# Optimization experiments

Measured on AMD Instinct MI355X. Metric: run time of the kernel, lower is better.

The kernel has to match this reference:

```python
import jax, jax.numpy as jnp
import numpy as np

N_NODES = 32768
N_EDGES = 524288
NODE_DIM = 128
HIDDEN = 256
EDGE_DIM = 32


def setup_inputs() -> dict:
    key = jax.random.key(0)
    ks = jax.random.split(key, 12)
    s = 0.05
    return {
        "h": jax.random.normal(ks[0], (N_NODES, NODE_DIM), jnp.float32),
        "x": jax.random.normal(ks[1], (N_NODES, 3), jnp.float32) * 10.0,
        "edge_index": jax.random.randint(ks[2], (2, N_EDGES), 0, N_NODES, dtype=jnp.int32).astype(jnp.int64),
        "edge_dist": jax.random.uniform(ks[3], (N_EDGES,), jnp.float32) * 15.0,
        # edge_mlp: Linear(1, edge_dim) -> SiLU -> Linear(edge_dim, edge_dim)
        "We1": jax.random.normal(ks[4], (1, EDGE_DIM), jnp.float32) * s,
        "be1": jnp.zeros((EDGE_DIM,), jnp.float32),
        "We2": jax.random.normal(ks[5], (EDGE_DIM, EDGE_DIM), jnp.float32) * s,
        "be2": jnp.zeros((EDGE_DIM,), jnp.float32),
        # node_mlp: Linear(2*node+edge, hidden) -> SiLU -> Linear(hidden, node)
        "Wn1": jax.random.normal(ks[6], (2 * NODE_DIM + EDGE_DIM, HIDDEN), jnp.float32) * s,
        "bn1": jnp.zeros((HIDDEN,), jnp.float32),
        "Wn2": jax.random.normal(ks[7], (HIDDEN, NODE_DIM), jnp.float32) * s,
        "bn2": jnp.zeros((NODE_DIM,), jnp.float32),
        # coord_mlp: Linear(2*node+edge, hidden) -> SiLU -> Linear(hidden, 1, bias=False)
        "Wc1": jax.random.normal(ks[8], (2 * NODE_DIM + EDGE_DIM, HIDDEN), jnp.float32) * s,
        "bc1": jnp.zeros((HIDDEN,), jnp.float32),
        "Wc2": jax.random.normal(ks[9], (HIDDEN, 1), jnp.float32) * s,
    }


def reference(h, x, edge_index, edge_dist,
              We1, be1, We2, be2,
              Wn1, bn1, Wn2, bn2,
              Wc1, bc1, Wc2):
    src, dst = edge_index[0], edge_index[1]
    n_nodes = h.shape[0]

    # edge_mlp on scalar distances -> [E, edge_dim]
    edge_attr = jax.nn.silu(edge_dist[:, None] @ We1 + be1) @ We2 + be2

    # per-edge message input: [E, 2*node_dim + edge_dim]
    m_input = jnp.concatenate([h[src], h[dst], edge_attr], axis=-1)

    # node messages and scatter-add onto destination nodes
    m = jax.nn.silu(m_input @ Wn1 + bn1) @ Wn2 + bn2          # [E, node_dim]
    h_agg = jax.ops.segment_sum(m, dst, num_segments=n_nodes)  # [N, node_dim]

    # equivariant coordinate update along normalized edge direction
    coord_weight = jax.nn.silu(m_input @ Wc1 + bc1) @ Wc2      # [E, 1]
    dir_vec = x[src] - x[dst]                                  # [E, 3]
    dir_len = jnp.maximum(jnp.linalg.norm(dir_vec, axis=-1, keepdims=True), 1e-8)
    coord_update = coord_weight * (dir_vec / dir_len)          # [E, 3]
    x_agg = jax.ops.segment_sum(coord_update, dst, num_segments=n_nodes)

    return h + h_agg, x + x_agg
```

## Files before the change

### kernel.cpp

```cpp
#include <hip/hip_runtime.h>
#include <math.h>

#define N_NODES 32768
#define N_EDGES 524288
#define NODE_DIM 128
#define HIDDEN 256
#define EDGE_DIM 32
#define TE 32
#define NBLK (N_EDGES / TE)
#define ASTR 296
#define HSTR 264
#define MSTR 132

typedef __attribute__((ext_vector_type(8))) short bf16x8;
typedef __attribute__((ext_vector_type(16))) float f32x16;

__device__ __forceinline__ float silu_f(float v) {
    float e = __expf(-v);
    return v * __builtin_amdgcn_rcpf(1.0f + e);
}

__device__ __forceinline__ unsigned short f2bf_rne(float f) {
    union { float f; unsigned int u; } v; v.f = f;
    return (unsigned short)((v.u + 0x7fffu + ((v.u >> 16) & 1u)) >> 16);
}
__device__ __forceinline__ unsigned int pk_rne(float a, float b) {
    return (unsigned int)f2bf_rne(a) | ((unsigned int)f2bf_rne(b) << 16);
}
__device__ __forceinline__ unsigned int pkbf(float a, float b) {
    union { float f; unsigned int u; } ua, ub; ua.f = a; ub.f = b;
    return __builtin_amdgcn_perm(ub.u + 0x8000u, ua.u + 0x8000u, 0x07060302u);
}
__device__ __forceinline__ unsigned short f2bf_hu(float f) {
    union { float f; unsigned int u; } v; v.f = f;
    return (unsigned short)((v.u + 0x8000u) >> 16);
}

__device__ __forceinline__ int detect_is64(const void* ei, int t) {
    const unsigned int* ew = (const unsigned int*)ei;
    unsigned int hiw = ew[2 * (t & 63) + 1];
    return (__ballot(hiw != 0u) == 0ULL) ? 1 : 0;
}

#define WS_BIAS_OFF 1024
#define WS_W1S_OFF  69632
#define WS_W2S_OFF  364544
#define WS_CNT_OFF  430080
#define WS_CUR_OFF  561152
#define WS_PERM_OFF 692224
#define WS_PART_OFF 2789376
#define WS_HBF_OFF  2790400
#define WS_HBF_END  (WS_HBF_OFF + N_NODES * NODE_DIM * 2)

#define SEG_CNT  32768
#define SEG_W1S  147456
#define SEG_W2S  32768
#define SEG_BIAS 512
#define SEG_OUT  1073152
#define SEG_HBF  524288
#define PREP_TOT (SEG_CNT + SEG_W1S + SEG_W2S + SEG_BIAS + SEG_OUT + SEG_HBF)

__global__ void prep_all_kernel(const float* __restrict__ h, const float* __restrict__ x,
                                const float* __restrict__ We2, const float* __restrict__ be2,
                                const float* __restrict__ Wn1, const float* __restrict__ bn1,
                                const float* __restrict__ Wn2,
                                const float* __restrict__ Wc1, const float* __restrict__ bc1,
                                float* __restrict__ out, float* __restrict__ biasC,
                                unsigned short* __restrict__ W1s, unsigned short* __restrict__ W2s,
                                int* __restrict__ counts, unsigned short* __restrict__ hbf) {
    int i = blockIdx.x * 256 + threadIdx.x;
    if (i < SEG_CNT) { counts[i] = 0; return; }
    i -= SEG_CNT;
    if (i < SEG_W1S) {
        int jj = i & 7, ln = (i >> 3) & 63, rest = i >> 9;
        int step = rest % 18, tile = rest / 18;
        int n = tile * 32 + (ln & 31);
        int k = step * 16 + ((ln >> 5) * 8) + jj;
        float v;
        if (k < 256) {
            v = (n < 256) ? Wn1[k * 256 + n] : Wc1[k * 256 + (n - 256)];
        } else {
            int j = k - 256;
            float s = 0.0f;
            #pragma unroll 8
            for (int q = 0; q < 32; ++q)
                s += We2[j * 32 + q] * ((n < 256) ? Wn1[(256 + q) * 256 + n]
                                                  : Wc1[(256 + q) * 256 + (n - 256)]);
            v = s;
        }
        W1s[i] = f2bf_rne(v);
        return;
    }
    i -= SEG_W1S;
    if (i < SEG_W2S) {
        int jj = i & 7, ln = (i >> 3) & 63, rest = i >> 9;
        int step = rest & 15, tile = rest >> 4;
        int d = tile * 32 + (ln & 31);
        int k = step * 16 + ((ln >> 5) * 8) + jj;
        W2s[i] = f2bf_rne(Wn2[k * 128 + d]);
        return;
    }
    i -= SEG_W2S;
    if (i < SEG_BIAS) {
        int n = i;
        float s = (n < 256) ? bn1[n] : bc1[n - 256];
        #pragma unroll 8
        for (int q = 0; q < 32; ++q)
            s += be2[q] * ((n < 256) ? Wn1[(256 + q) * 256 + n]
                                     : Wc1[(256 + q) * 256 + (n - 256)]);
        biasC[n] = s;
        return;
    }
    i -= SEG_BIAS;
    if (i < SEG_OUT) {
        const int NH4 = N_NODES * NODE_DIM / 4;
        const float4* h4 = (const float4*)h;
        const float4* x4 = (const float4*)x;
        ((float4*)out)[i] = (i < NH4) ? h4[i] : x4[i - NH4];
        return;
    }
    i -= SEG_OUT;
    if (hbf != nullptr && i < SEG_HBF) {
        const float4* p = (const float4*)&h[i * 8];
        float4 v0 = p[0], v1 = p[1];
        uint4 o = make_uint4(pk_rne(v0.x, v0.y), pk_rne(v0.z, v0.w),
                             pk_rne(v1.x, v1.y), pk_rne(v1.z, v1.w));
        *(uint4*)&hbf[i * 8] = o;
    }
}

__global__ void hist_kernel(const void* __restrict__ ei, int* __restrict__ counts) {
    int is64 = detect_is64(ei, threadIdx.x);
    int e = blockIdx.x * 256 + threadIdx.x;
    int dst = is64 ? (int)((const long long*)ei)[N_EDGES + e]
                   : ((const int*)ei)[N_EDGES + e];
    atomicAdd(&counts[dst], 1);
}

__global__ __launch_bounds__(256)
void scanA_kernel(const int* __restrict__ counts, int* __restrict__ partials) {
    __shared__ int red[256];
    const int t = threadIdx.x;
    const int b = blockIdx.x;
    red[t] = counts[b * 256 + t];
    __syncthreads();
    #pragma unroll
    for (int s = 128; s > 0; s >>= 1) {
        if (t < s) red[t] += red[t + s];
        __syncthreads();
    }
    if (t == 0) partials[b] = red[0];
}

__global__ __launch_bounds__(256)
void scanC_kernel(const int* __restrict__ counts, const int* __restrict__ partials,
                  int* __restrict__ cursor) {
    __shared__ int pb[128];
    __shared__ int loc[256];
    const int t = threadIdx.x;
    const int b = blockIdx.x;
    if (t < 128) pb[t] = partials[t];
    int c = counts[b * 256 + t];
    loc[t] = c;
    __syncthreads();
    if (t == 0) {
        int s = 0;
        for (int j = 0; j < 128; ++j) { int v = pb[j]; pb[j] = s; s += v; }
    }
    #pragma unroll
    for (int d = 1; d < 256; d <<= 1) {
        int v = (t >= d) ? loc[t - d] : 0;
        __syncthreads();
        loc[t] += v;
        __syncthreads();
    }
    cursor[b * 256 + t] = pb[b] + loc[t] - c;
}

__global__ void place_kernel(const void* __restrict__ ei,
                             int* __restrict__ cursor, int* __restrict__ perm) {
    int is64 = detect_is64(ei, threadIdx.x);
    int e = blockIdx.x * 256 + threadIdx.x;
    int dst = is64 ? (int)((const long long*)ei)[N_EDGES + e]
                   : ((const int*)ei)[N_EDGES + e];
    int pos = atomicAdd(&cursor[dst], 1);
    perm[pos] = e;
}

__global__ __launch_bounds__(256, 5)
void egnn_mfma_kernel(const float* __restrict__ h, const float* __restrict__ x,
                      const void* __restrict__ ei, const float* __restrict__ dist,
                      const float* __restrict__ We1, const float* __restrict__ be1,
                      const float* __restrict__ bn2, const float* __restrict__ Wc2,
                      const float* __restrict__ biasC,
                      const unsigned short* __restrict__ W1s,
                      const unsigned short* __restrict__ W2s,
                      const int* __restrict__ perm,
                      const unsigned short* __restrict__ hbf,
                      float* __restrict__ out)
{
    __shared__ unsigned short smA[TE * ASTR];
    __shared__ int sidx[TE], didx[TE], eidx[TE];
    __shared__ float cw_s[TE];
    __shared__ float cxyz[3 * TE];

    unsigned short* smH = smA;
    float* smM = (float*)smA;

    const int t = threadIdx.x;
    const int lane = t & 63;
    const int wv = t >> 6;
    const int lo = lane & 31;
    const int hi = lane >> 5;
    const int swz = ((blockIdx.x & 7) * (NBLK / 8)) + (blockIdx.x >> 3);
    const int ebase = swz * TE;
    const int is64 = detect_is64(ei, t);

    if (t < 2 * TE) {
        int e = t & (TE - 1);
        int eid = perm[ebase + e];
        int which = t >> 5;
        long long pos = (long long)which * N_EDGES + eid;
        int idx = is64 ? (int)((const long long*)ei)[pos] : ((const int*)ei)[pos];
        if (which == 0) { sidx[e] = idx; eidx[e] = eid; }
        else didx[e] = idx;
        if (t < TE) cw_s[t] = 0.0f;
    }
    __syncthreads();

    if (hbf != nullptr) {
        #pragma unroll
        for (int it = 0; it < 4; ++it) {
            int id = it * 256 + t;
            int g = id & 15;
            int half = (id >> 4) & 1;
            int e = id >> 5;
            int node = half ? didx[e] : sidx[e];
            uint4 v = *(const uint4*)&hbf[node * NODE_DIM + 8 * g];
            *(uint4*)&smA[e * ASTR + half * NODE_DIM + 8 * g] = v;
        }
    } else {
        #pragma unroll
        for (int it = 0; it < 4; ++it) {
            int id = it * 256 + t;
            int g8 = id & 15;
            int half = (id >> 4) & 1;
            int e = id >> 5;
            int node = half ? didx[e] : sidx[e];
            const float4* p = (const float4*)&h[node * NODE_DIM + 8 * g8];
            float4 v0 = p[0], v1 = p[1];
            unsigned int a0 = pkbf(v0.x, v0.y), a1 = pkbf(v0.z, v0.w);
            unsigned int a2 = pkbf(v1.x, v1.y), a3 = pkbf(v1.z, v1.w);
            *(uint4*)&smA[e * ASTR + half * NODE_DIM + 8 * g8] = make_uint4(a0, a1, a2, a3);
        }
    }
    {
        int e = t >> 3;
        int j4 = (t & 7) * 4;
        float d = dist[eidx[e]];
        float s0 = silu_f(d * We1[j4 + 0] + be1[j4 + 0]);
        float s1 = silu_f(d * We1[j4 + 1] + be1[j4 + 1]);
        float s2 = silu_f(d * We1[j4 + 2] + be1[j4 + 2]);
        float s3 = silu_f(d * We1[j4 + 3] + be1[j4 + 3]);
        *(uint2*)&smA[e * ASTR + 2 * NODE_DIM + j4] = make_uint2(pkbf(s0, s1), pkbf(s2, s3));
    }
    if (t < TE) {
        int s = sidx[t], dn = didx[t];
        float dx = x[s * 3 + 0] - x[dn * 3 + 0];
        float dy = x[s * 3 + 1] - x[dn * 3 + 1];
        float dz = x[s * 3 + 2] - x[dn * 3 + 2];
        float len = fmaxf(sqrtf(dx * dx + dy * dy + dz * dz), 1e-8f);
        float inv = 1.0f / len;
        cxyz[t] = dx * inv; cxyz[TE + t] = dy * inv; cxyz[2 * TE + t] = dz * inv;
    }
    __syncthreads();

    const int rowbase = 4 * hi;

    {
        f32x16 c0, c1;
        {
            float b0 = biasC[256 + wv * 32 + lo];
            float b1 = biasC[256 + (wv + 4) * 32 + lo];
            #pragma unroll
            for (int r = 0; r < 16; ++r) { c0[r] = b0; c1[r] = b1; }
        }
        {
            const int ao = lo * ASTR + hi * 8;
            const int TS = 18 * 64 * 8;
            const int q0 = (8 + wv) * TS + lane * 8;
            const int q1 = (12 + wv) * TS + lane * 8;
            bf16x8 p0[2], p1[2];
            p0[0] = *(const bf16x8*)&W1s[q0];
            p1[0] = *(const bf16x8*)&W1s[q1];
            #pragma unroll
            for (int step = 0; step < 18; ++step) {
                const int cur = step & 1, nxt = cur ^ 1;
                if (step + 1 < 18) {
                    p0[nxt] = *(const bf16x8*)&W1s[q0 + (step + 1) * 512];
                    p1[nxt] = *(const bf16x8*)&W1s[q1 + (step + 1) * 512];
                }
                bf16x8 f = *(const bf16x8*)&smA[ao + step * 16];
                c0 = __builtin_amdgcn_mfma_f32_32x32x16_bf16(f, p0[cur], c0, 0, 0, 0);
                c1 = __builtin_amdgcn_mfma_f32_32x32x16_bf16(f, p1[cur], c1, 0, 0, 0);
            }
        }
        float w0 = Wc2[wv * 32 + lo];
        float w1 = Wc2[(wv + 4) * 32 + lo];
        float p[16];
        #pragma unroll
        for (int r = 0; r < 16; ++r)
            p[r] = silu_f(c0[r]) * w0 + silu_f(c1[r]) * w1;
        #pragma unroll
        for (int off = 1; off < 32; off <<= 1) {
            #pragma unroll
            for (int r = 0; r < 16; ++r) p[r] += __shfl_xor(p[r], off);
        }
        if (lo == 0) {
            #pragma unroll
            for (int r = 0; r < 16; ++r)
                atomicAdd(&cw_s[(r & 3) + 8 * (r >> 2) + rowbase], p[r]);
        }
    }

    f32x16 a0, a1;
    {
        float b0 = biasC[wv * 32 + lo];
        float b1 = biasC[(wv + 4) * 32 + lo];
        #pragma unroll
        for (int r = 0; r < 16; ++r) { a0[r] = b0; a1[r] = b1; }
        const int ao = lo * ASTR + hi * 8;
        const int TS = 18 * 64 * 8;
        const int q0 = (wv) * TS + lane * 8;
        const int q1 = (wv + 4) * TS + lane * 8;
        bf16x8 p0[2], p1[2];
        p0[0] = *(const bf16x8*)&W1s[q0];
        p1[0] = *(const bf16x8*)&W1s[q1];
        #pragma unroll
        for (int step = 0; step < 18; ++step) {
            const int cur = step & 1, nxt = cur ^ 1;
            if (step + 1 < 18) {
                p0[nxt] = *(const bf16x8*)&W1s[q0 + (step + 1) * 512];
                p1[nxt] = *(const bf16x8*)&W1s[q1 + (step + 1) * 512];
            }
            bf16x8 f = *(const bf16x8*)&smA[ao + step * 16];
            a0 = __builtin_amdgcn_mfma_f32_32x32x16_bf16(f, p0[cur], a0, 0, 0, 0);
            a1 = __builtin_amdgcn_mfma_f32_32x32x16_bf16(f, p1[cur], a1, 0, 0, 0);
        }
    }
    __syncthreads();

    {
        const int jb0 = (wv    ) * 32 + lo;
        const int jb1 = (wv + 4) * 32 + lo;
        #pragma unroll
        for (int r = 0; r < 16; ++r) {
            int er = (r & 3) + 8 * (r >> 2) + rowbase;
            smH[er * HSTR + jb0] = f2bf_hu(silu_f(a0[r]));
            smH[er * HSTR + jb1] = f2bf_hu(silu_f(a1[r]));
        }
    }
    if (t < TE) {
        float w = cw_s[t];
        cxyz[t] *= w; cxyz[TE + t] *= w; cxyz[2 * TE + t] *= w;
    }
    __syncthreads();

    {
        const int d = wv * 32 + lo;
        f32x16 acc;
        float bb = bn2[d];
        #pragma unroll
        for (int r = 0; r < 16; ++r) acc[r] = bb;
        const int hoff = lo * HSTR + hi * 8;
        const int wb = wv * (16 * 64 * 8) + lane * 8;
        bf16x8 bs[2];
        bs[0] = *(const bf16x8*)&W2s[wb];
        #pragma unroll
        for (int step = 0; step < 16; ++step) {
            const int cur = step & 1, nxt = cur ^ 1;
            if (step + 1 < 16)
                bs[nxt] = *(const bf16x8*)&W2s[wb + (step + 1) * 512];
            bf16x8 af = *(const bf16x8*)&smH[hoff + step * 16];
            acc = __builtin_amdgcn_mfma_f32_32x32x16_bf16(af, bs[cur], acc, 0, 0, 0);
        }
        __syncthreads();
        #pragma unroll
        for (int r = 0; r < 16; ++r) {
            int er = (r & 3) + 8 * (r >> 2) + rowbase;
            smM[er * MSTR + d] = acc[r];
        }
    }
    __syncthreads();

    {
        const int g = t >> 5;
        const int d4 = (t & 31) * 4;
        for (int e0 = g; e0 < TE; e0 += 8) {
            if (e0 > 0 && didx[e0] == didx[e0 - 1]) continue;
            float4 s = *(const float4*)&smM[e0 * MSTR + d4];
            int er = e0 + 1;
            while (er < TE && didx[er] == didx[e0]) {
                float4 v = *(const float4*)&smM[er * MSTR + d4];
                s.x += v.x; s.y += v.y; s.z += v.z; s.w += v.w;
                ++er;
            }
            float* dp = &out[didx[e0] * NODE_DIM + d4];
            if (e0 > 0 && er < TE) {
                float4 cur = *(const float4*)dp;
                cur.x += s.x; cur.y += s.y; cur.z += s.z; cur.w += s.w;
                *(float4*)dp = cur;
            } else {
                atomicAdd(dp + 0, s.x); atomicAdd(dp + 1, s.y);
                atomicAdd(dp + 2, s.z); atomicAdd(dp + 3, s.w);
            }
        }
    }
    if (t < TE) {
        int e0 = t;
        if (e0 == 0 || didx[e0] != didx[e0 - 1]) {
            float sx = cxyz[e0], sy = cxyz[TE + e0], sz = cxyz[2 * TE + e0];
            int er = e0 + 1;
            while (er < TE && didx[er] == didx[e0]) {
                sx += cxyz[er]; sy += cxyz[TE + er]; sz += cxyz[2 * TE + er];
                ++er;
            }
            float* xo = out + N_NODES * NODE_DIM + didx[e0] * 3;
            if (e0 > 0 && er < TE) {
                xo[0] += sx; xo[1] += sy; xo[2] += sz;
            } else {
                atomicAdd(xo + 0, sx); atomicAdd(xo + 1, sy); atomicAdd(xo + 2, sz);
            }
        }
    }
}

extern "C" void kernel_launch(void* const* d_in, const int* in_sizes, int n_in,
                              void* d_out, int out_size, void* d_ws, size_t ws_size,
                              hipStream_t stream) {
    const float* h    = (const float*)d_in[0];
    const float* x    = (const float*)d_in[1];
    const void*  ei   = d_in[2];
    const float* dist = (const float*)d_in[3];
    const float* We1  = (const float*)d_in[4];
    const float* be1  = (const float*)d_in[5];
    const float* We2  = (const float*)d_in[6];
    const float* be2  = (const float*)d_in[7];
    const float* Wn1  = (const float*)d_in[8];
    const float* bn1  = (const float*)d_in[9];
    const float* Wn2  = (const float*)d_in[10];
    const float* bn2  = (const float*)d_in[11];
    const float* Wc1  = (const float*)d_in[12];
    const float* bc1  = (const float*)d_in[13];
    const float* Wc2  = (const float*)d_in[14];
    float* out = (float*)d_out;

    float* biasC = (float*)((char*)d_ws + WS_BIAS_OFF);
    unsigned short* W1s = (unsigned short*)((char*)d_ws + WS_W1S_OFF);
    unsigned short* W2s = (unsigned short*)((char*)d_ws + WS_W2S_OFF);
    int* counts   = (int*)((char*)d_ws + WS_CNT_OFF);
    int* cursor   = (int*)((char*)d_ws + WS_CUR_OFF);
    int* perm     = (int*)((char*)d_ws + WS_PERM_OFF);
    int* partials = (int*)((char*)d_ws + WS_PART_OFF);
    unsigned short* hbf = (ws_size >= (size_t)WS_HBF_END)
                        ? (unsigned short*)((char*)d_ws + WS_HBF_OFF) : nullptr;

    prep_all_kernel<<<PREP_TOT / 256, 256, 0, stream>>>(
        h, x, We2, be2, Wn1, bn1, Wn2, Wc1, bc1,
        out, biasC, W1s, W2s, counts, hbf);

    hist_kernel<<<N_EDGES / 256, 256, 0, stream>>>(ei, counts);
    scanA_kernel<<<128, 256, 0, stream>>>(counts, partials);
    scanC_kernel<<<128, 256, 0, stream>>>(counts, partials, cursor);
    place_kernel<<<N_EDGES / 256, 256, 0, stream>>>(ei, cursor, perm);

    egnn_mfma_kernel<<<NBLK, 256, 0, stream>>>(
        h, x, ei, dist, We1, be1, bn2, Wc2, biasC, W1s, W2s, perm, hbf, out);
}
```

Measured before the change: 477.7 us.

## Fuse histogram into prep kernel, merge scan passes, raise MFMA occupancy bound

The destination histogram now runs inside the prep kernel, and counts are zeroed with a memset instead of a prep segment. The two-pass scan becomes one kernel in which each block recomputes all 128 block partials from counts. Together this removes two launches and their serial dependencies. The main EGNN kernel's launch bound goes from 5 to 6 blocks per SM, which may add register pressure or spills.

Result: faster. 467.9 us (-2.1%).

```diff
diff --git a/kernel.cpp b/kernel.cpp
--- a/kernel.cpp
+++ b/kernel.cpp
@@ -52,25 +52,32 @@
 #define WS_HBF_OFF  2790400
 #define WS_HBF_END  (WS_HBF_OFF + N_NODES * NODE_DIM * 2)
 
-#define SEG_CNT  32768
+#define SEG_HIST 524288
 #define SEG_W1S  147456
 #define SEG_W2S  32768
 #define SEG_BIAS 512
 #define SEG_OUT  1073152
 #define SEG_HBF  524288
-#define PREP_TOT (SEG_CNT + SEG_W1S + SEG_W2S + SEG_BIAS + SEG_OUT + SEG_HBF)
-
-__global__ void prep_all_kernel(const float* __restrict__ h, const float* __restrict__ x,
-                                const float* __restrict__ We2, const float* __restrict__ be2,
-                                const float* __restrict__ Wn1, const float* __restrict__ bn1,
-                                const float* __restrict__ Wn2,
-                                const float* __restrict__ Wc1, const float* __restrict__ bc1,
-                                float* __restrict__ out, float* __restrict__ biasC,
-                                unsigned short* __restrict__ W1s, unsigned short* __restrict__ W2s,
-                                int* __restrict__ counts, unsigned short* __restrict__ hbf) {
+#define PREP_TOT (SEG_HIST + SEG_W1S + SEG_W2S + SEG_BIAS + SEG_OUT + SEG_HBF)
+
+__global__ void prep_hist_kernel(const float* __restrict__ h, const float* __restrict__ x,
+                                 const void* __restrict__ ei,
+                                 const float* __restrict__ We2, const float* __restrict__ be2,
+                                 const float* __restrict__ Wn1, const float* __restrict__ bn1,
+                                 const float* __restrict__ Wn2,
+                                 const float* __restrict__ Wc1, const float* __restrict__ bc1,
+                                 float* __restrict__ out, float* __restrict__ biasC,
+                                 unsigned short* __restrict__ W1s, unsigned short* __restrict__ W2s,
+                                 int* __restrict__ counts, unsigned short* __restrict__ hbf) {
     int i = blockIdx.x * 256 + threadIdx.x;
-    if (i < SEG_CNT) { counts[i] = 0; return; }
-    i -= SEG_CNT;
+    if (i < SEG_HIST) {
+        int is64 = detect_is64(ei, threadIdx.x);
+        int dst = is64 ? (int)((const long long*)ei)[N_EDGES + i]
+                       : ((const int*)ei)[N_EDGES + i];
+        atomicAdd(&counts[dst], 1);
+        return;
+    }
+    i -= SEG_HIST;
     if (i < SEG_W1S) {
         int jj = i & 7, ln = (i >> 3) & 63, rest = i >> 9;
         int step = rest % 18, tile = rest / 18;
@@ -129,37 +136,19 @@
     }
 }
 
-__global__ void hist_kernel(const void* __restrict__ ei, int* __restrict__ counts) {
-    int is64 = detect_is64(ei, threadIdx.x);
-    int e = blockIdx.x * 256 + threadIdx.x;
-    int dst = is64 ? (int)((const long long*)ei)[N_EDGES + e]
-                   : ((const int*)ei)[N_EDGES + e];
-    atomicAdd(&counts[dst], 1);
-}
-
 __global__ __launch_bounds__(256)
-void scanA_kernel(const int* __restrict__ counts, int* __restrict__ partials) {
-    __shared__ int red[256];
-    const int t = threadIdx.x;
-    const int b = blockIdx.x;
-    red[t] = counts[b * 256 + t];
-    __syncthreads();
-    #pragma unroll
-    for (int s = 128; s > 0; s >>= 1) {
-        if (t < s) red[t] += red[t + s];
-        __syncthreads();
-    }
-    if (t == 0) partials[b] = red[0];
-}
-
-__global__ __launch_bounds__(256)
-void scanC_kernel(const int* __restrict__ counts, const int* __restrict__ partials,
-                  int* __restrict__ cursor) {
+void scan_fused_kernel(const int* __restrict__ counts, int* __restrict__ cursor) {
     __shared__ int pb[128];
     __shared__ int loc[256];
     const int t = threadIdx.x;
     const int b = blockIdx.x;
-    if (t < 128) pb[t] = partials[t];
+    if (t < 128) {
+        const int4* c4 = (const int4*)(counts + t * 256);
+        int s = 0;
+        #pragma unroll 8
+        for (int i = 0; i < 64; ++i) { int4 v = c4[i]; s += v.x + v.y + v.z + v.w; }
+        pb[t] = s;
+    }
     int c = counts[b * 256 + t];
     loc[t] = c;
     __syncthreads();
@@ -187,7 +176,7 @@
     perm[pos] = e;
 }
 
-__global__ __launch_bounds__(256, 5)
+__global__ __launch_bounds__(256, 6)
 void egnn_mfma_kernel(const float* __restrict__ h, const float* __restrict__ x,
                       const void* __restrict__ ei, const float* __restrict__ dist,
                       const float* __restrict__ We1, const float* __restrict__ be1,
@@ -461,17 +450,16 @@
     int* counts   = (int*)((char*)d_ws + WS_CNT_OFF);
     int* cursor   = (int*)((char*)d_ws + WS_CUR_OFF);
     int* perm     = (int*)((char*)d_ws + WS_PERM_OFF);
-    int* partials = (int*)((char*)d_ws + WS_PART_OFF);
     unsigned short* hbf = (ws_size >= (size_t)WS_HBF_END)
                         ? (unsigned short*)((char*)d_ws + WS_HBF_OFF) : nullptr;
 
-    prep_all_kernel<<<PREP_TOT / 256, 256, 0, stream>>>(
-        h, x, We2, be2, Wn1, bn1, Wn2, Wc1, bc1,
+    hipMemsetAsync(counts, 0, N_NODES * sizeof(int), stream);
+
+    prep_hist_kernel<<<PREP_TOT / 256, 256, 0, stream>>>(
+        h, x, ei, We2, be2, Wn1, bn1, Wn2, Wc1, bc1,
         out, biasC, W1s, W2s, counts, hbf);
 
-    hist_kernel<<<N_EDGES / 256, 256, 0, stream>>>(ei, counts);
-    scanA_kernel<<<128, 256, 0, stream>>>(counts, partials);
-    scanC_kernel<<<128, 256, 0, stream>>>(counts, partials, cursor);
+    scan_fused_kernel<<<128, 256, 0, stream>>>(counts, cursor);
     place_kernel<<<N_EDGES / 256, 256, 0, stream>>>(ei, cursor, perm);
 
     egnn_mfma_kernel<<<NBLK, 256, 0, stream>>>(
```
